# Performance work log

Hardware: AMD Instinct MI355X
Metric: run time of the kernel (lower is better)

Reference implementation:

```python
import jax, jax.numpy as jnp
import numpy as np

NUM_HEADS = 16

def setup_inputs() -> dict:
    key = jax.random.key(0)
    ks = jax.random.split(key, 5)
    B, L, H = 4, 1024, 1024
    s = 0.02
    return {
        'x': jax.random.normal(ks[0], (B, L, H), jnp.float32),
        'Wq': jax.random.normal(ks[1], (H, H), jnp.float32) * s,
        'Wkv_short': jax.random.normal(ks[2], (H, 2 * H), jnp.float32) * s,
        'Wkv_long': jax.random.normal(ks[3], (H, 2 * H), jnp.float32) * s,
        'Wo': jax.random.normal(ks[4], (H, H), jnp.float32) * s,
        'mix_weight': jnp.float32(0.5),
        'decay_factor': jnp.float32(0.95),
    }

def _heads(t, B, L, nh, hd):
    # [B, L, H] -> [B, nh, L, hd]
    return t.reshape(B, L, nh, hd).transpose(0, 2, 1, 3)

def _attention(q, k, v, bias):
    # q,k,v: [B, nh, L, hd]; bias: [L, L] or None
    hd = q.shape[-1]
    scores = jnp.einsum('bhqd,bhkd->bhqk', q, k) / jnp.sqrt(jnp.float32(hd))
    if bias is not None:
        scores = scores + bias[None, None]
    attn = jax.nn.softmax(scores, axis=-1)
    return jnp.einsum('bhqk,bhkd->bhqd', attn, v)

def reference(x, Wq, Wkv_short, Wkv_long, Wo, mix_weight, decay_factor):
    B, L, H = x.shape
    nh = NUM_HEADS
    hd = H // nh
    q = _heads(x @ Wq, B, L, nh, hd)
    kv_s = x @ Wkv_short
    k_s = _heads(kv_s[..., :H], B, L, nh, hd)
    v_s = _heads(kv_s[..., H:], B, L, nh, hd)
    pos = jnp.arange(L, dtype=jnp.float32)
    decay_bias = -jnp.abs(pos[None, :] - pos[:, None]) * (1.0 - decay_factor)
    out_short = _attention(q, k_s, v_s, decay_bias)
    kv_l = x @ Wkv_long
    k_l = _heads(kv_l[..., :H], B, L, nh, hd)
    v_l = _heads(kv_l[..., H:], B, L, nh, hd)
    out_long = _attention(q, k_l, v_l, None)
    alpha = jax.nn.sigmoid(mix_weight)
    out = alpha * out_short + (1.0 - alpha) * out_long
    out = out.transpose(0, 2, 1, 3).reshape(B, L, H)
    return out @ Wo
```

## Files before the change

### kernel.cpp

```cpp
#include <hip/hip_runtime.h>
#include <hip/hip_bf16.h>
#include <math.h>
#include <stdint.h>

typedef unsigned short u16;
typedef __attribute__((ext_vector_type(8))) short bf16x8;
typedef __attribute__((ext_vector_type(4))) float f32x4;
typedef __attribute__((ext_vector_type(4))) unsigned short u16x4;
typedef __attribute__((ext_vector_type(4))) unsigned int uint32x4;

#define MFMA_BF16(A, B, C) __builtin_amdgcn_mfma_f32_16x16x32_bf16((A), (B), (C), 0, 0, 0)

__device__ __forceinline__ void async16(const void* g, const void* l) {
    __builtin_amdgcn_global_load_lds(
        (const __attribute__((address_space(1))) unsigned int*)(uintptr_t)g,
        (__attribute__((address_space(3))) unsigned int*)(uintptr_t)l, 16, 0, 0);
}

__device__ __forceinline__ u16 f2bf(float f) {
    unsigned u = __float_as_uint(f);
    u += 0x7fffu + ((u >> 16) & 1u);
    return (u16)(u >> 16);
}

__device__ __forceinline__ unsigned pack2(float a, float b) {
    __hip_bfloat162 h = __float22bfloat162_rn(float2{a, b});
    return *reinterpret_cast<unsigned*>(&h);
}

__device__ __forceinline__ float bf2f(u16 v) {
    unsigned u = ((unsigned)v) << 16;
    return __uint_as_float(u);
}

__device__ __forceinline__ bf16x8 mk_frag(unsigned w0, unsigned w1,
                                          unsigned w2, unsigned w3) {
    uint32x4 u = {w0, w1, w2, w3};
    return __builtin_bit_cast(bf16x8, u);
}

__global__ __launch_bounds__(256) void cvt_x(const float* __restrict__ x,
                                             u16* __restrict__ xb) {
    int i = blockIdx.x * 256 + threadIdx.x;
    float4 v = ((const float4*)x)[i];
    u16x4 o = {f2bf(v.x), f2bf(v.y), f2bf(v.z), f2bf(v.w)};
    ((u16x4*)xb)[i] = o;
}

__global__ __launch_bounds__(256) void cvt_w_all(
    const float* __restrict__ Wq, const float* __restrict__ Wks,
    const float* __restrict__ Wkl, const float* __restrict__ Wo,
    u16* __restrict__ wqt, u16* __restrict__ wkst,
    u16* __restrict__ wklt, u16* __restrict__ wot)
{
    __shared__ float tile[32][33];
    int x = blockIdx.x;
    const float* W; u16* Wt; int N, nb;
    if (x < 32)       { W = Wq;  Wt = wqt;  N = 1024; nb = x * 32; }
    else if (x < 96)  { W = Wks; Wt = wkst; N = 2048; nb = (x - 32) * 32; }
    else if (x < 160) { W = Wkl; Wt = wklt; N = 2048; nb = (x - 96) * 32; }
    else              { W = Wo;  Wt = wot;  N = 1024; nb = (x - 160) * 32; }
    int kb = blockIdx.y * 32;
    int t = threadIdx.x;
    int r = t >> 3, c4 = (t & 7) * 4;
    float4 v = *(const float4*)&W[(size_t)(kb + r) * N + nb + c4];
    tile[r][c4] = v.x; tile[r][c4 + 1] = v.y;
    tile[r][c4 + 2] = v.z; tile[r][c4 + 3] = v.w;
    __syncthreads();
    u16x4 o = {f2bf(tile[c4 + 0][r]), f2bf(tile[c4 + 1][r]),
               f2bf(tile[c4 + 2][r]), f2bf(tile[c4 + 3][r])};
    *(u16x4*)&Wt[(size_t)(nb + r) * 1024 + kb + c4] = o;
}

__global__ __launch_bounds__(256, 4) void gemm_proj(
    const u16* __restrict__ A, const u16* __restrict__ wq,
    const u16* __restrict__ wks, const u16* __restrict__ wkl,
    u16* __restrict__ qd, u16* __restrict__ ksd, u16* __restrict__ vsd,
    u16* __restrict__ kld, u16* __restrict__ vld)
{
    __shared__ u16 Alds[2][128][32];
    __shared__ u16 Blds[2][128][32];

    const int cx = blockIdx.x;
    const int rowBase = blockIdx.y * 128;

    const u16* Bt; u16* dK; u16* dV; int colBase; float osc = 1.0f;
    bool ktype;
    if (cx < 8)       { Bt = wq;  colBase = cx * 128;        dK = qd;  dV = nullptr;
                        osc = 0.18033688f; ktype = true; }
    else if (cx < 24) { Bt = wks; colBase = (cx - 8) * 128;  dK = ksd; dV = vsd;
                        ktype = (cx < 16); }
    else              { Bt = wkl; colBase = (cx - 24) * 128; dK = kld; dV = vld;
                        ktype = (cx < 32); }

    const int t = threadIdx.x;
    const int l = t & 63, w = t >> 6;
    const int wm = w & 1, wn = w >> 1;
    const int lc = l & 15, lr4 = l >> 4;

    f32x4 acc[4][4];
#pragma unroll
    for (int i = 0; i < 4; i++)
#pragma unroll
        for (int j = 0; j < 4; j++) acc[i][j] = (f32x4){0.f, 0.f, 0.f, 0.f};

    const int srow = w * 32 + (l >> 2);
    const int sc8  = (((l & 3) ^ ((l >> 2) & 3)) * 8);
    const u16* Ag = A  + (size_t)(rowBase + srow) * 1024 + sc8;
    const u16* Bg = Bt + (size_t)(colBase + srow) * 1024 + sc8;
    const int sw = (lc & 3);

    auto stage = [&](int kt, int buf) {
        const int ko = kt * 32;
        async16(Ag + ko,         &Alds[buf][w * 32][0]);
        async16(Ag + ko + 16384, &Alds[buf][w * 32 + 16][0]);
        async16(Bg + ko,         &Blds[buf][w * 32][0]);
        async16(Bg + ko + 16384, &Blds[buf][w * 32 + 16][0]);
    };

    stage(0, 0);
    __syncthreads();

    for (int kt = 0; kt < 32; ++kt) {
        const int cur = kt & 1;
        if (kt + 1 < 32) stage(kt + 1, cur ^ 1);

        const u16 (*Lm)[32] = ktype ? Blds[cur] : Alds[cur];
        const u16 (*Ln)[32] = ktype ? Alds[cur] : Blds[cur];

        bf16x8 af[4], bf[4];
#pragma unroll
        for (int mt = 0; mt < 4; ++mt)
            af[mt] = *(const bf16x8*)&Lm[wm * 64 + mt * 16 + lc][(lr4 ^ sw) * 8];
#pragma unroll
        for (int nt = 0; nt < 4; ++nt)
            bf[nt] = *(const bf16x8*)&Ln[wn * 64 + nt * 16 + lc][(lr4 ^ sw) * 8];
#pragma unroll
        for (int mt = 0; mt < 4; ++mt)
#pragma unroll
            for (int nt = 0; nt < 4; ++nt)
                acc[mt][nt] = MFMA_BF16(af[mt], bf[nt], acc[mt][nt]);

        __syncthreads();
    }

    if (ktype) {
#pragma unroll
        for (int mt = 0; mt < 4; ++mt)
#pragma unroll
            for (int nt = 0; nt < 4; ++nt) {
                int f   = colBase + wm * 64 + mt * 16 + lr4 * 4;
                int tok = rowBase + wn * 64 + nt * 16 + lc;
                int b = tok >> 10, tk = tok & 1023;
                int head = (f >> 6) & 15, d = f & 63;
                u16x4 pv = {f2bf(acc[mt][nt][0] * osc), f2bf(acc[mt][nt][1] * osc),
                            f2bf(acc[mt][nt][2] * osc), f2bf(acc[mt][nt][3] * osc)};
                *(u16x4*)&dK[((size_t)(b * 16 + head) * 1024 + tk) * 64 + d] = pv;
            }
    } else {
#pragma unroll
        for (int mt = 0; mt < 4; ++mt)
#pragma unroll
            for (int nt = 0; nt < 4; ++nt) {
                int gr0 = rowBase + wm * 64 + mt * 16 + lr4 * 4;
                int gc0 = colBase + wn * 64 + nt * 16;
                int head = gc0 >> 6;
                int b = gr0 >> 10, tok = gr0 & 1023;
                int tokp = (tok & ~31) | (((tok >> 2) & 3) << 3) |
                           (((tok >> 4) & 1) << 2);
                int d = (gc0 & 63) + lc;
                u16x4 pv = {f2bf(acc[mt][nt][0]), f2bf(acc[mt][nt][1]),
                            f2bf(acc[mt][nt][2]), f2bf(acc[mt][nt][3])};
                *(u16x4*)&dV[((size_t)(b * 16 + head - 16) * 64 + d) * 1024 +
                             tokp] = pv;
            }
    }
}

__global__ __launch_bounds__(256) void gemm_out(
    const u16* __restrict__ Aattn, const u16* __restrict__ Bwot,
    float* __restrict__ dst)
{
    __shared__ u16 Alds[2][64][32];
    __shared__ u16 Blds[2][128][32];
    const int t = threadIdx.x;
    const int l = t & 63, w = t >> 6;
    const int wm = w & 1, wn = w >> 1;

    const int wg  = blockIdx.y * 8 + blockIdx.x;
    const int swz = (wg & 7) * 64 + (wg >> 3);
    const int rowBase = (swz >> 3) * 64;
    const int colBase = (swz & 7) * 128;

    const int lc = l & 15, lr4 = l >> 4;

    f32x4 acc[4][2];
#pragma unroll
    for (int i = 0; i < 4; i++)
#pragma unroll
        for (int j = 0; j < 2; j++) acc[i][j] = (f32x4){0.f, 0.f, 0.f, 0.f};

    const int sl  = l >> 2;
    const int sc8 = (((l & 3) ^ (sl & 3)) * 8);
    const u16* Ag = Aattn + (size_t)(rowBase + w * 16 + sl) * 1024 + sc8;
    const u16* Bg = Bwot  + (size_t)(colBase + w * 32 + sl) * 1024 + sc8;
    const int sw = (lc & 3);

    auto stage = [&](int kt, int buf) {
        const int ko = kt * 32;
        async16(Ag + ko,         &Alds[buf][w * 16][0]);
        async16(Bg + ko,         &Blds[buf][w * 32][0]);
        async16(Bg + ko + 16384, &Blds[buf][w * 32 + 16][0]);
    };

    stage(0, 0);
    __syncthreads();

    for (int kt = 0; kt < 32; ++kt) {
        const int cur = kt & 1;
        if (kt + 1 < 32) stage(kt + 1, cur ^ 1);

        bf16x8 af[4], bf[2];
#pragma unroll
        for (int mt = 0; mt < 4; ++mt)
            af[mt] = *(const bf16x8*)&Blds[cur][wm * 64 + mt * 16 + lc][(lr4 ^ sw) * 8];
#pragma unroll
        for (int nt = 0; nt < 2; ++nt)
            bf[nt] = *(const bf16x8*)&Alds[cur][wn * 32 + nt * 16 + lc][(lr4 ^ sw) * 8];
#pragma unroll
        for (int mt = 0; mt < 4; ++mt)
#pragma unroll
            for (int nt = 0; nt < 2; ++nt)
                acc[mt][nt] = MFMA_BF16(af[mt], bf[nt], acc[mt][nt]);

        __syncthreads();
    }

#pragma unroll
    for (int mt = 0; mt < 4; ++mt)
#pragma unroll
        for (int nt = 0; nt < 2; ++nt) {
            int f   = colBase + wm * 64 + mt * 16 + lr4 * 4;
            int tok = rowBase + wn * 32 + nt * 16 + lc;
            float4 v = {acc[mt][nt][0], acc[mt][nt][1],
                        acc[mt][nt][2], acc[mt][nt][3]};
            *(float4*)&dst[(size_t)tok * 1024 + f] = v;
        }
}

__global__ __launch_bounds__(256, 4) void attn_mfma(
    const u16* __restrict__ Q, const u16* __restrict__ Ksb,
    const u16* __restrict__ Vsb, const u16* __restrict__ Klb,
    const u16* __restrict__ Vlb, const float* __restrict__ decayf,
    u16* __restrict__ Os, u16* __restrict__ Ol)
{
    __shared__ __align__(16) u16 Kt[2][2][64][32];
    __shared__ __align__(16) u16 Vt[2][2][64][32];

    const int t = threadIdx.x;
    const int l = t & 63, w = t >> 6;
    const int lc = l & 15, lr4 = l >> 4;
    const int h = blockIdx.x, qt = blockIdx.y;
    const int b = blockIdx.z >> 1, branch = blockIdx.z & 1;
    const size_t bh = (size_t)(b * 16 + h);
    const int qbase = qt * 128;
    const u16* Qg = Q + bh * (1024 * 64);
    const u16* Kg = (branch ? Klb : Ksb) + bh * (1024 * 64);
    const u16* Vg = (branch ? Vlb : Vsb) + bh * (64 * 1024);
    u16* outp = branch ? Ol : Os;

    const int sl = l >> 2;
    const int sc = (((l & 3) ^ ((l >> 3) & 3)) * 8);
    const int swr = (lc >> 1) & 3;

    int ktLo = 0, ktHi = 16;
    if (branch == 0) {
        ktLo = qt * 2 - 7; if (ktLo < 0) ktLo = 0;
        ktHi = qt * 2 + 9; if (ktHi > 16) ktHi = 16;
    }

    bf16x8 aQ[2][2];
#pragma unroll
    for (int qg = 0; qg < 2; ++qg)
#pragma unroll
        for (int kh = 0; kh < 2; ++kh)
            aQ[qg][kh] = *(const bf16x8*)&Qg[
                (size_t)(qbase + w * 32 + qg * 16 + lc) * 64 + kh * 32 + lr4 * 8];

    auto stage = [&](int kt, int buf) {
#pragma unroll
        for (int i = 0; i < 4; i++) {
            int id = w * 4 + i;
            int kh = (id >> 2) & 1, ch = id & 3;
            if (id < 8)
                async16(Kg + (size_t)(kt * 64 + ch * 16 + sl) * 64 + kh * 32 + sc,
                        &Kt[buf][kh][ch * 16][0]);
            else
                async16(Vg + (size_t)(ch * 16 + sl) * 1024 + kt * 64 + kh * 32 + sc,
                        &Vt[buf][kh][ch * 16][0]);
        }
    };

    stage(ktLo, 0);
    __syncthreads();

    const float C2 = (1.0f - decayf[0]) * 1.44269504f;
    const float qf = (float)(qbase + w * 32 + lc);

    f32x4 sumv[2] = {(f32x4){0.f, 0.f, 0.f, 0.f}, (f32x4){0.f, 0.f, 0.f, 0.f}};
    f32x4 o[2][4];
#pragma unroll
    for (int qg = 0; qg < 2; ++qg)
#pragma unroll
        for (int dt = 0; dt < 4; ++dt) o[qg][dt] = (f32x4){0.f, 0.f, 0.f, 0.f};

    for (int kt = ktLo, it = 0; kt < ktHi; ++kt, ++it) {
        const int cur = it & 1;
        if (kt + 1 < ktHi) stage(kt + 1, cur ^ 1);

        bf16x8 ak[4][2];
#pragma unroll
        for (int nt = 0; nt < 4; ++nt) {
            ak[nt][0] = *(const bf16x8*)&Kt[cur][0][nt * 16 + lc][(lr4 ^ swr) * 8];
            ak[nt][1] = *(const bf16x8*)&Kt[cur][1][nt * 16 + lc][(lr4 ^ swr) * 8];
        }

        unsigned pw[2][8];
#pragma unroll
        for (int qg = 0; qg < 2; ++qg) {
            const float d0 = qf + (float)(qg * 16 - kt * 64 - lr4 * 4);
            f32x4 s[4];
#pragma unroll
            for (int nt = 0; nt < 4; ++nt) {
                if (branch == 0) {
                    float dd = d0 - (float)(nt * 16);
                    s[nt] = (f32x4){-fabsf(dd) * C2,
                                    -fabsf(dd - 1.0f) * C2,
                                    -fabsf(dd - 2.0f) * C2,
                                    -fabsf(dd - 3.0f) * C2};
                } else {
                    s[nt] = (f32x4){0.f, 0.f, 0.f, 0.f};
                }
                s[nt] = MFMA_BF16(ak[nt][0], aQ[qg][0], s[nt]);
                s[nt] = MFMA_BF16(ak[nt][1], aQ[qg][1], s[nt]);
            }
#pragma unroll
            for (int nt = 0; nt < 4; ++nt) {
                float p0 = __builtin_amdgcn_exp2f(s[nt][0]);
                float p1 = __builtin_amdgcn_exp2f(s[nt][1]);
                float p2 = __builtin_amdgcn_exp2f(s[nt][2]);
                float p3 = __builtin_amdgcn_exp2f(s[nt][3]);
                sumv[qg][0] += p0; sumv[qg][1] += p1;
                sumv[qg][2] += p2; sumv[qg][3] += p3;
                pw[qg][nt * 2]     = pack2(p0, p1);
                pw[qg][nt * 2 + 1] = pack2(p2, p3);
            }
        }

#pragma unroll
        for (int dt = 0; dt < 4; ++dt) {
            bf16x8 v0 = *(const bf16x8*)&Vt[cur][0][dt * 16 + lc][(lr4 ^ swr) * 8];
            bf16x8 v1 = *(const bf16x8*)&Vt[cur][1][dt * 16 + lc][(lr4 ^ swr) * 8];
#pragma unroll
            for (int qg = 0; qg < 2; ++qg) {
                bf16x8 pb0 = mk_frag(pw[qg][0], pw[qg][1], pw[qg][2], pw[qg][3]);
                bf16x8 pb1 = mk_frag(pw[qg][4], pw[qg][5], pw[qg][6], pw[qg][7]);
                o[qg][dt] = MFMA_BF16(v0, pb0, o[qg][dt]);
                o[qg][dt] = MFMA_BF16(v1, pb1, o[qg][dt]);
            }
        }

        __syncthreads();
    }

#pragma unroll
    for (int qg = 0; qg < 2; ++qg) {
        float s = (sumv[qg][0] + sumv[qg][1]) + (sumv[qg][2] + sumv[qg][3]);
        s += __shfl_xor(s, 16);
        s += __shfl_xor(s, 32);
        float inv = 1.0f / s;
        int qrow = qbase + w * 32 + qg * 16 + lc;
        u16* op = outp + ((size_t)(b * 1024) + qrow) * 1024 + h * 64;
#pragma unroll
        for (int dt = 0; dt < 4; ++dt) {
            uint2 w2 = {pack2(o[qg][dt][0] * inv, o[qg][dt][1] * inv),
                        pack2(o[qg][dt][2] * inv, o[qg][dt][3] * inv)};
            *(uint2*)&op[dt * 16 + lr4 * 4] = w2;
        }
    }
}

__global__ __launch_bounds__(256) void mix_kernel(
    const u16* __restrict__ Os, const u16* __restrict__ Ol,
    const float* __restrict__ mixw, u16* __restrict__ dst)
{
    const float a = 1.0f / (1.0f + __expf(-mixw[0]));
    int i = blockIdx.x * 256 + threadIdx.x;
    uint4 s = ((const uint4*)Os)[i];
    uint4 l = ((const uint4*)Ol)[i];
    unsigned su[4] = {s.x, s.y, s.z, s.w};
    unsigned lu[4] = {l.x, l.y, l.z, l.w};
    unsigned ou[4];
#pragma unroll
    for (int k = 0; k < 4; ++k) {
        float s0 = bf2f((u16)su[k]), s1 = bf2f((u16)(su[k] >> 16));
        float l0 = bf2f((u16)lu[k]), l1 = bf2f((u16)(lu[k] >> 16));
        ou[k] = pack2(l0 + a * (s0 - l0), l1 + a * (s1 - l1));
    }
    ((uint4*)dst)[i] = make_uint4(ou[0], ou[1], ou[2], ou[3]);
}

extern "C" void kernel_launch(void* const* d_in, const int* in_sizes, int n_in,
                              void* d_out, int out_size, void* d_ws, size_t ws_size,
                              hipStream_t stream) {
    const float* x      = (const float*)d_in[0];
    const float* Wq     = (const float*)d_in[1];
    const float* Wkvs   = (const float*)d_in[2];
    const float* Wkvl   = (const float*)d_in[3];
    const float* Wo     = (const float*)d_in[4];
    const float* mixw   = (const float*)d_in[5];
    const float* decayf = (const float*)d_in[6];

    const size_t M1 = 1024 * 1024;
    u16* ws    = (u16*)d_ws;
    u16* xb    = ws;
    u16* wqt   = xb + 4 * M1;
    u16* wkvst = wqt + 1 * M1;
    u16* wkvlt = wkvst + 2 * M1;
    u16* wot   = wkvlt + 2 * M1;
    u16* qb    = wot + 1 * M1;
    u16* ksb   = qb + 4 * M1;
    u16* vsb   = ksb + 4 * M1;
    u16* klb   = vsb + 4 * M1;
    u16* vlb   = klb + 4 * M1;
    u16* attnb = vlb + 4 * M1;
    u16* osb   = xb;
    u16* olb   = wqt;

    cvt_x<<<4096, 256, 0, stream>>>(x, xb);
    cvt_w_all<<<dim3(192, 32), 256, 0, stream>>>(Wq, Wkvs, Wkvl, Wo,
                                                 wqt, wkvst, wkvlt, wot);
    gemm_proj<<<dim3(40, 32), 256, 0, stream>>>(xb, wqt, wkvst, wkvlt,
                                                qb, ksb, vsb, klb, vlb);
    attn_mfma<<<dim3(16, 8, 8), 256, 0, stream>>>(qb, ksb, vsb, klb, vlb,
                                                  decayf, osb, olb);
    mix_kernel<<<2048, 256, 0, stream>>>(osb, olb, mixw, attnb);
    gemm_out<<<dim3(8, 64), 256, 0, stream>>>(attnb, wot, (float*)d_out);
}
```

Baseline: 226.9 us.

## Fuse both attention branches and the sigmoid mix into one attention kernel

```diff
diff --git a/kernel.cpp b/kernel.cpp
--- a/kernel.cpp
+++ b/kernel.cpp
@@ -248,11 +248,11 @@
         }
 }
 
-__global__ __launch_bounds__(256, 4) void attn_mfma(
+__global__ __launch_bounds__(256, 3) void attn_mfma(
     const u16* __restrict__ Q, const u16* __restrict__ Ksb,
     const u16* __restrict__ Vsb, const u16* __restrict__ Klb,
     const u16* __restrict__ Vlb, const float* __restrict__ decayf,
-    u16* __restrict__ Os, u16* __restrict__ Ol)
+    const float* __restrict__ mixw, u16* __restrict__ dst)
 {
     __shared__ __align__(16) u16 Kt[2][2][64][32];
     __shared__ __align__(16) u16 Vt[2][2][64][32];
@@ -260,25 +260,15 @@
     const int t = threadIdx.x;
     const int l = t & 63, w = t >> 6;
     const int lc = l & 15, lr4 = l >> 4;
-    const int h = blockIdx.x, qt = blockIdx.y;
-    const int b = blockIdx.z >> 1, branch = blockIdx.z & 1;
+    const int h = blockIdx.x, qt = blockIdx.y, b = blockIdx.z;
     const size_t bh = (size_t)(b * 16 + h);
     const int qbase = qt * 128;
     const u16* Qg = Q + bh * (1024 * 64);
-    const u16* Kg = (branch ? Klb : Ksb) + bh * (1024 * 64);
-    const u16* Vg = (branch ? Vlb : Vsb) + bh * (64 * 1024);
-    u16* outp = branch ? Ol : Os;
 
     const int sl = l >> 2;
     const int sc = (((l & 3) ^ ((l >> 3) & 3)) * 8);
     const int swr = (lc >> 1) & 3;
 
-    int ktLo = 0, ktHi = 16;
-    if (branch == 0) {
-        ktLo = qt * 2 - 7; if (ktLo < 0) ktLo = 0;
-        ktHi = qt * 2 + 9; if (ktHi > 16) ktHi = 16;
-    }
-
     bf16x8 aQ[2][2];
 #pragma unroll
     for (int qg = 0; qg < 2; ++qg)
@@ -287,127 +277,139 @@
             aQ[qg][kh] = *(const bf16x8*)&Qg[
                 (size_t)(qbase + w * 32 + qg * 16 + lc) * 64 + kh * 32 + lr4 * 8];
 
-    auto stage = [&](int kt, int buf) {
-#pragma unroll
-        for (int i = 0; i < 4; i++) {
-            int id = w * 4 + i;
-            int kh = (id >> 2) & 1, ch = id & 3;
-            if (id < 8)
-                async16(Kg + (size_t)(kt * 64 + ch * 16 + sl) * 64 + kh * 32 + sc,
-                        &Kt[buf][kh][ch * 16][0]);
-            else
-                async16(Vg + (size_t)(ch * 16 + sl) * 1024 + kt * 64 + kh * 32 + sc,
-                        &Vt[buf][kh][ch * 16][0]);
+    const float C2 = (1.0f - decayf[0]) * 1.44269504f;
+    const float alpha = 1.0f / (1.0f + __expf(-mixw[0]));
+    const float qf = (float)(qbase + w * 32 + lc);
+
+    uint2 w0[2][4];
+
+#pragma unroll
+    for (int br = 0; br < 2; ++br) {
+        const u16* Kg = (br ? Klb : Ksb) + bh * (1024 * 64);
+        const u16* Vg = (br ? Vlb : Vsb) + bh * (64 * 1024);
+
+        int ktLo = 0, ktHi = 16;
+        if (br == 0) {
+            ktLo = qt * 2 - 7; if (ktLo < 0) ktLo = 0;
+            ktHi = qt * 2 + 9; if (ktHi > 16) ktHi = 16;
         }
-    };
-
-    stage(ktLo, 0);
-    __syncthreads();
-
-    const float C2 = (1.0f - decayf[0]) * 1.44269504f;
-    const float qf = (float)(qbase + w * 32 + lc);
-
-    f32x4 sumv[2] = {(f32x4){0.f, 0.f, 0.f, 0.f}, (f32x4){0.f, 0.f, 0.f, 0.f}};
-    f32x4 o[2][4];
-#pragma unroll
-    for (int qg = 0; qg < 2; ++qg)
-#pragma unroll
-        for (int dt = 0; dt < 4; ++dt) o[qg][dt] = (f32x4){0.f, 0.f, 0.f, 0.f};
-
-    for (int kt = ktLo, it = 0; kt < ktHi; ++kt, ++it) {
-        const int cur = it & 1;
-        if (kt + 1 < ktHi) stage(kt + 1, cur ^ 1);
-
-        bf16x8 ak[4][2];
-#pragma unroll
-        for (int nt = 0; nt < 4; ++nt) {
-            ak[nt][0] = *(const bf16x8*)&Kt[cur][0][nt * 16 + lc][(lr4 ^ swr) * 8];
-            ak[nt][1] = *(const bf16x8*)&Kt[cur][1][nt * 16 + lc][(lr4 ^ swr) * 8];
+
+        auto stage = [&](int kt, int buf) {
+#pragma unroll
+            for (int i = 0; i < 4; i++) {
+                int id = w * 4 + i;
+                int kh = (id >> 2) & 1, ch = id & 3;
+                if (id < 8)
+                    async16(Kg + (size_t)(kt * 64 + ch * 16 + sl) * 64 + kh * 32 + sc,
+                            &Kt[buf][kh][ch * 16][0]);
+                else
+                    async16(Vg + (size_t)(ch * 16 + sl) * 1024 + kt * 64 + kh * 32 + sc,
+                            &Vt[buf][kh][ch * 16][0]);
+            }
+        };
+
+        f32x4 sumv[2] = {(f32x4){0.f, 0.f, 0.f, 0.f},
+                         (f32x4){0.f, 0.f, 0.f, 0.f}};
+        f32x4 o[2][4];
+#pragma unroll
+        for (int qg = 0; qg < 2; ++qg)
+#pragma unroll
+            for (int dt = 0; dt < 4; ++dt) o[qg][dt] = (f32x4){0.f, 0.f, 0.f, 0.f};
+
+        stage(ktLo, 0);
+        __syncthreads();
+
+        for (int kt = ktLo, it = 0; kt < ktHi; ++kt, ++it) {
+            const int cur = it & 1;
+            if (kt + 1 < ktHi) stage(kt + 1, cur ^ 1);
+
+            bf16x8 ak[4][2];
+#pragma unroll
+            for (int nt = 0; nt < 4; ++nt) {
+                ak[nt][0] = *(const bf16x8*)&Kt[cur][0][nt * 16 + lc][(lr4 ^ swr) * 8];
+                ak[nt][1] = *(const bf16x8*)&Kt[cur][1][nt * 16 + lc][(lr4 ^ swr) * 8];
+            }
+
+            unsigned pw[2][8];
+#pragma unroll
+            for (int qg = 0; qg < 2; ++qg) {
+                const float d0 = qf + (float)(qg * 16 - kt * 64 - lr4 * 4);
+                f32x4 s[4];
+#pragma unroll
+                for (int nt = 0; nt < 4; ++nt) {
+                    if (br == 0) {
+                        float dd = d0 - (float)(nt * 16);
+                        s[nt] = (f32x4){-fabsf(dd) * C2,
+                                        -fabsf(dd - 1.0f) * C2,
+                                        -fabsf(dd - 2.0f) * C2,
+                                        -fabsf(dd - 3.0f) * C2};
+                    } else {
+                        s[nt] = (f32x4){0.f, 0.f, 0.f, 0.f};
+                    }
+                    s[nt] = MFMA_BF16(ak[nt][0], aQ[qg][0], s[nt]);
+                    s[nt] = MFMA_BF16(ak[nt][1], aQ[qg][1], s[nt]);
+                }
+#pragma unroll
+                for (int nt = 0; nt < 4; ++nt) {
+                    float p0 = __builtin_amdgcn_exp2f(s[nt][0]);
+                    float p1 = __builtin_amdgcn_exp2f(s[nt][1]);
+                    float p2 = __builtin_amdgcn_exp2f(s[nt][2]);
+                    float p3 = __builtin_amdgcn_exp2f(s[nt][3]);
+                    sumv[qg][0] += p0; sumv[qg][1] += p1;
+                    sumv[qg][2] += p2; sumv[qg][3] += p3;
+                    pw[qg][nt * 2]     = pack2(p0, p1);
+                    pw[qg][nt * 2 + 1] = pack2(p2, p3);
+                }
+            }
+
+#pragma unroll
+            for (int dt = 0; dt < 4; ++dt) {
+                bf16x8 v0 = *(const bf16x8*)&Vt[cur][0][dt * 16 + lc][(lr4 ^ swr) * 8];
+                bf16x8 v1 = *(const bf16x8*)&Vt[cur][1][dt * 16 + lc][(lr4 ^ swr) * 8];
+#pragma unroll
+                for (int qg = 0; qg < 2; ++qg) {
+                    bf16x8 pb0 = mk_frag(pw[qg][0], pw[qg][1], pw[qg][2], pw[qg][3]);
+                    bf16x8 pb1 = mk_frag(pw[qg][4], pw[qg][5], pw[qg][6], pw[qg][7]);
+                    o[qg][dt] = MFMA_BF16(v0, pb0, o[qg][dt]);
+                    o[qg][dt] = MFMA_BF16(v1, pb1, o[qg][dt]);
+                }
+            }
+
+            __syncthreads();
         }
 
-        unsigned pw[2][8];
 #pragma unroll
         for (int qg = 0; qg < 2; ++qg) {
-            const float d0 = qf + (float)(qg * 16 - kt * 64 - lr4 * 4);
-            f32x4 s[4];
-#pragma unroll
-            for (int nt = 0; nt < 4; ++nt) {
-                if (branch == 0) {
-                    float dd = d0 - (float)(nt * 16);
-                    s[nt] = (f32x4){-fabsf(dd) * C2,
-                                    -fabsf(dd - 1.0f) * C2,
-                                    -fabsf(dd - 2.0f) * C2,
-                                    -fabsf(dd - 3.0f) * C2};
-                } else {
-                    s[nt] = (f32x4){0.f, 0.f, 0.f, 0.f};
+            float s = (sumv[qg][0] + sumv[qg][1]) + (sumv[qg][2] + sumv[qg][3]);
+            s += __shfl_xor(s, 16);
+            s += __shfl_xor(s, 32);
+            float inv = 1.0f / s;
+            if (br == 0) {
+#pragma unroll
+                for (int dt = 0; dt < 4; ++dt)
+                    w0[qg][dt] = uint2{
+                        pack2(o[qg][dt][0] * inv, o[qg][dt][1] * inv),
+                        pack2(o[qg][dt][2] * inv, o[qg][dt][3] * inv)};
+            } else {
+                int qrow = qbase + w * 32 + qg * 16 + lc;
+                u16* op = dst + ((size_t)(b * 1024) + qrow) * 1024 + h * 64;
+#pragma unroll
+                for (int dt = 0; dt < 4; ++dt) {
+                    float s0 = bf2f((u16)(w0[qg][dt].x));
+                    float s1 = bf2f((u16)(w0[qg][dt].x >> 16));
+                    float s2 = bf2f((u16)(w0[qg][dt].y));
+                    float s3 = bf2f((u16)(w0[qg][dt].y >> 16));
+                    float l0 = o[qg][dt][0] * inv, l1 = o[qg][dt][1] * inv;
+                    float l2 = o[qg][dt][2] * inv, l3 = o[qg][dt][3] * inv;
+                    uint2 w2 = {pack2(l0 + alpha * (s0 - l0),
+                                      l1 + alpha * (s1 - l1)),
+                                pack2(l2 + alpha * (s2 - l2),
+                                      l3 + alpha * (s3 - l3))};
+                    *(uint2*)&op[dt * 16 + lr4 * 4] = w2;
                 }
-                s[nt] = MFMA_BF16(ak[nt][0], aQ[qg][0], s[nt]);
-                s[nt] = MFMA_BF16(ak[nt][1], aQ[qg][1], s[nt]);
-            }
-#pragma unroll
-            for (int nt = 0; nt < 4; ++nt) {
-                float p0 = __builtin_amdgcn_exp2f(s[nt][0]);
-                float p1 = __builtin_amdgcn_exp2f(s[nt][1]);
-                float p2 = __builtin_amdgcn_exp2f(s[nt][2]);
-                float p3 = __builtin_amdgcn_exp2f(s[nt][3]);
-                sumv[qg][0] += p0; sumv[qg][1] += p1;
-                sumv[qg][2] += p2; sumv[qg][3] += p3;
-                pw[qg][nt * 2]     = pack2(p0, p1);
-                pw[qg][nt * 2 + 1] = pack2(p2, p3);
-            }
-        }
-
-#pragma unroll
-        for (int dt = 0; dt < 4; ++dt) {
-            bf16x8 v0 = *(const bf16x8*)&Vt[cur][0][dt * 16 + lc][(lr4 ^ swr) * 8];
-            bf16x8 v1 = *(const bf16x8*)&Vt[cur][1][dt * 16 + lc][(lr4 ^ swr) * 8];
-#pragma unroll
-            for (int qg = 0; qg < 2; ++qg) {
-                bf16x8 pb0 = mk_frag(pw[qg][0], pw[qg][1], pw[qg][2], pw[qg][3]);
-                bf16x8 pb1 = mk_frag(pw[qg][4], pw[qg][5], pw[qg][6], pw[qg][7]);
-                o[qg][dt] = MFMA_BF16(v0, pb0, o[qg][dt]);
-                o[qg][dt] = MFMA_BF16(v1, pb1, o[qg][dt]);
-            }
-        }
-
-        __syncthreads();
-    }
-
-#pragma unroll
-    for (int qg = 0; qg < 2; ++qg) {
-        float s = (sumv[qg][0] + sumv[qg][1]) + (sumv[qg][2] + sumv[qg][3]);
-        s += __shfl_xor(s, 16);
-        s += __shfl_xor(s, 32);
-        float inv = 1.0f / s;
-        int qrow = qbase + w * 32 + qg * 16 + lc;
-        u16* op = outp + ((size_t)(b * 1024) + qrow) * 1024 + h * 64;
-#pragma unroll
-        for (int dt = 0; dt < 4; ++dt) {
-            uint2 w2 = {pack2(o[qg][dt][0] * inv, o[qg][dt][1] * inv),
-                        pack2(o[qg][dt][2] * inv, o[qg][dt][3] * inv)};
-            *(uint2*)&op[dt * 16 + lr4 * 4] = w2;
+            }
         }
     }
-}
-
-__global__ __launch_bounds__(256) void mix_kernel(
-    const u16* __restrict__ Os, const u16* __restrict__ Ol,
-    const float* __restrict__ mixw, u16* __restrict__ dst)
-{
-    const float a = 1.0f / (1.0f + __expf(-mixw[0]));
-    int i = blockIdx.x * 256 + threadIdx.x;
-    uint4 s = ((const uint4*)Os)[i];
-    uint4 l = ((const uint4*)Ol)[i];
-    unsigned su[4] = {s.x, s.y, s.z, s.w};
-    unsigned lu[4] = {l.x, l.y, l.z, l.w};
-    unsigned ou[4];
-#pragma unroll
-    for (int k = 0; k < 4; ++k) {
-        float s0 = bf2f((u16)su[k]), s1 = bf2f((u16)(su[k] >> 16));
-        float l0 = bf2f((u16)lu[k]), l1 = bf2f((u16)(lu[k] >> 16));
-        ou[k] = pack2(l0 + a * (s0 - l0), l1 + a * (s1 - l1));
-    }
-    ((uint4*)dst)[i] = make_uint4(ou[0], ou[1], ou[2], ou[3]);
 }
 
 extern "C" void kernel_launch(void* const* d_in, const int* in_sizes, int n_in,
@@ -434,16 +436,13 @@
     u16* klb   = vsb + 4 * M1;
     u16* vlb   = klb + 4 * M1;
     u16* attnb = vlb + 4 * M1;
-    u16* osb   = xb;
-    u16* olb   = wqt;
 
     cvt_x<<<4096, 256, 0, stream>>>(x, xb);
     cvt_w_all<<<dim3(192, 32), 256, 0, stream>>>(Wq, Wkvs, Wkvl, Wo,
                                                  wqt, wkvst, wkvlt, wot);
     gemm_proj<<<dim3(40, 32), 256, 0, stream>>>(xb, wqt, wkvst, wkvlt,
                                                 qb, ksb, vsb, klb, vlb);
-    attn_mfma<<<dim3(16, 8, 8), 256, 0, stream>>>(qb, ksb, vsb, klb, vlb,
-                                                  decayf, osb, olb);
-    mix_kernel<<<2048, 256, 0, stream>>>(osb, olb, mixw, attnb);
+    attn_mfma<<<dim3(16, 8, 4), 256, 0, stream>>>(qb, ksb, vsb, klb, vlb,
+                                                  decayf, mixw, attnb);
     gemm_out<<<dim3(8, 64), 256, 0, stream>>>(attnb, wot, (float*)d_out);
 }
```

Result: faster. 218.7 us (-3.6%).
